# Kernel optimization log

Measured on AMD Instinct MI355X. Metric: run time of the kernel, lower is better.

The kernel has to match this reference:

```python
import math
import jax, jax.numpy as jnp
import numpy as np

H = 8
DIM = 256
HD = DIM // H
SCALE = math.sqrt(HD)
EPS = 1e-16


def _segment_softmax(scores, dst, num_nodes):
    # scores: [E, H], dst: [E] -> softmax over edges sharing the same dst
    m = jax.ops.segment_max(scores, dst, num_segments=num_nodes)  # [N, H]
    m = jnp.where(jnp.isfinite(m), m, 0.0)  # empty segments -> -inf -> 0
    e = jnp.exp(scores - m[dst])
    s = jax.ops.segment_sum(e, dst, num_segments=num_nodes)  # [N, H]
    return e / (s[dst] + EPS)


def _graph_attention(x, edges, wq, bq, wk, bk, wv, bv, wo, bo):
    # x: [N, DIM]; edges: [2, E] (src, dst). Dropout is identity (eval mode).
    N = x.shape[0]
    Q = (x @ wq + bq).reshape(N, H, HD)
    K = (x @ wk + bk).reshape(N, H, HD)
    V = (x @ wv + bv).reshape(N, H, HD)
    src, dst = edges[0], edges[1]
    scores = jnp.einsum('ehd,ehd->eh', Q[dst], K[src]) / SCALE  # [E, H]
    attn = _segment_softmax(scores, dst, N)  # [E, H]
    msgs = V[src] * attn[:, :, None]  # [E, H, HD]
    out = jax.ops.segment_sum(msgs, dst, num_segments=N).reshape(N, DIM)
    return out @ wo + bo


def _linear_params(key, fan_in, fan_out):
    k1, k2 = jax.random.split(key)
    bound = 1.0 / math.sqrt(fan_in)
    w = jax.random.uniform(k1, (fan_in, fan_out), minval=-bound, maxval=bound, dtype=jnp.float32)
    b = jax.random.uniform(k2, (fan_out,), minval=-bound, maxval=bound, dtype=jnp.float32)
    return w, b


def setup_inputs() -> dict:
    key = jax.random.key(0)
    ks = jax.random.split(key, 12)
    n_slot, n_dom = 20000, 1000
    e_slot, e_dom = 320000, 16000
    inp = {
        'slot_x': jax.random.normal(ks[0], (n_slot, DIM), dtype=jnp.float32),
        'domain_x': jax.random.normal(ks[1], (n_dom, DIM), dtype=jnp.float32),
        'slot_edges': jax.random.randint(ks[2], (2, e_slot), 0, n_slot, dtype=jnp.int32),
        'domain_edges': jax.random.randint(ks[3], (2, e_dom), 0, n_dom, dtype=jnp.int32),
    }
    names = ['wq', 'wk', 'wv', 'wo']
    for i, nm in enumerate(names):
        w, b = _linear_params(ks[4 + i], DIM, DIM)
        inp[f'slot_{nm}'] = w
        inp[f'slot_{nm}_b'] = b
    for i, nm in enumerate(names):
        w, b = _linear_params(ks[8 + i], DIM, DIM)
        inp[f'dom_{nm}'] = w
        inp[f'dom_{nm}_b'] = b
    return inp


def reference(slot_x, domain_x, slot_edges, domain_edges,
              slot_wq, slot_wq_b, slot_wk, slot_wk_b, slot_wv, slot_wv_b, slot_wo, slot_wo_b,
              dom_wq, dom_wq_b, dom_wk, dom_wk_b, dom_wv, dom_wv_b, dom_wo, dom_wo_b):
    # slot branch: self-attention on slot graph + identity residual
    slot_out = _graph_attention(slot_x, slot_edges,
                                slot_wq, slot_wq_b, slot_wk, slot_wk_b,
                                slot_wv, slot_wv_b, slot_wo, slot_wo_b) + slot_x
    # domain branch
    dom_out = _graph_attention(domain_x, domain_edges,
                               dom_wq, dom_wq_b, dom_wk, dom_wk_b,
                               dom_wv, dom_wv_b, dom_wo, dom_wo_b) + domain_x
    return slot_out, dom_out
```

## Files before the change

### kernel.cpp

```cpp
#include <hip/hip_runtime.h>
#include <hip/hip_bf16.h>

#define DIM 256
#define INV_SCALE 0.17677669529663687f
#define SM_EPS 1e-16f
#define CAP 64

typedef unsigned short ushortT;
typedef unsigned int uintT;
typedef __attribute__((ext_vector_type(8))) __bf16 bf16x8;
typedef __attribute__((ext_vector_type(4))) float f32x4;

__device__ __forceinline__ float bf2f(ushortT u) {
    return __uint_as_float(((uintT)u) << 16);
}
__device__ __forceinline__ ushortT f2bf(float f) {
    uintT u = __float_as_uint(f);
    u += 0x7FFFu + ((u >> 16) & 1u);
    return (ushortT)(u >> 16);
}

struct WPack { const void* w[8]; const void* b[8]; };

__device__ __forceinline__ bool sniff_m16(const ushortT* __restrict__ x) {
    int lane = threadIdx.x & 63;
    ushortT u = x[lane * 2];
    int e = (u >> 7) & 0xFF;
    bool sane = ((u & 0x7FFFu) == 0) || (e >= 0x66 && e <= 0x90);
    unsigned long long m = __ballot(sane);
    return __popcll(m) >= 32;
}

__global__ __launch_bounds__(256) void megaA(
        const void* __restrict__ xs, const void* __restrict__ xd,
        const ushortT* __restrict__ sniff_src,
        ushortT* __restrict__ xb_s, ushortT* __restrict__ xb_d,
        WPack pk, ushortT* __restrict__ wT, float* __restrict__ biasF,
        int* __restrict__ flagWs,
        const int* __restrict__ src_s, const int* __restrict__ dst_s,
        const int* __restrict__ src_d, const int* __restrict__ dst_d,
        int* __restrict__ cnt_s, int* __restrict__ cnt_d,
        int* __restrict__ col_s, int* __restrict__ col_d,
        int Es_, int Ed_, int nSc,
        int n4s, int n4d, int nA0, int nA1)
{
    const int bid = blockIdx.x;
    const int t = threadIdx.x;

    if (bid < nSc) {
        const int idx = bid * 256 + t;
        if (idx < Es_) {
            const int dv = dst_s[idx];
            const int pos = atomicAdd(&cnt_s[dv], 1);
            if (pos < CAP) col_s[(size_t)dv * CAP + pos] = src_s[idx];
        } else {
            const int e = idx - Es_;
            if (e < Ed_) {
                const int dv = dst_d[e];
                const int pos = atomicAdd(&cnt_d[dv], 1);
                if (pos < CAP) col_d[(size_t)dv * CAP + pos] = src_d[e];
            }
        }
        return;
    }
    const bool m16 = sniff_m16(sniff_src);
    const int li2 = bid - nSc;

    if (li2 < nA0 + nA1) {
        const bool d = li2 >= nA0;
        const int li = d ? li2 - nA0 : li2;
        const int n4 = d ? n4d : n4s;
        const int i = li * 256 + t;
        if (i >= n4) return;
        const void* x = d ? xd : xs;
        ushortT* xb = d ? xb_d : xb_s;
        if (m16) {
            ((ushort4*)xb)[i] = ((const ushort4*)x)[i];
        } else {
            float4 v = ((const float4*)x)[i];
            ushort4 o2;
            o2.x = f2bf(v.x); o2.y = f2bf(v.y); o2.z = f2bf(v.z); o2.w = f2bf(v.w);
            ((ushort4*)xb)[i] = o2;
        }
    } else if (li2 < nA0 + nA1 + 128) {
        __shared__ float sh[64][65];
        const int r0 = li2 - (nA0 + nA1);
        const int which = r0 >> 4;
        const int tile = r0 & 15;
        const int tr = tile >> 2, tc = tile & 3;
        const void* w = pk.w[which];
        const int tx = t & 63, tg = t >> 6;
        #pragma unroll
        for (int i = 0; i < 16; ++i) {
            const int r = i * 4 + tg;
            const size_t si = (size_t)(tr * 64 + r) * 256 + tc * 64 + tx;
            sh[r][tx] = m16 ? bf2f(((const ushortT*)w)[si]) : ((const float*)w)[si];
        }
        __syncthreads();
        ushortT* o = wT + (size_t)which * 65536;
        #pragma unroll
        for (int i = 0; i < 16; ++i) {
            const int r = i * 4 + tg;
            o[(size_t)(tc * 64 + r) * 256 + tr * 64 + tx] = f2bf(sh[tx][r]);
        }
    } else if (li2 < nA0 + nA1 + 136) {
        const int which = li2 - (nA0 + nA1 + 128);
        const void* b = pk.b[which];
        float v = m16 ? bf2f(((const ushortT*)b)[t]) : ((const float*)b)[t];
        biasF[which * 256 + t] = v;
    } else {
        if (t == 0) *flagWs = m16 ? 1 : 0;
    }
}

__global__ __launch_bounds__(256) void megaB(
        const ushortT* __restrict__ xb_s, const ushortT* __restrict__ xb_d,
        const ushortT* __restrict__ wT, const float* __restrict__ biasF,
        ushortT* __restrict__ qkv_s, ushortT* __restrict__ qkv_d,
        size_t zss, size_t zsd, int Ms, int Md, int nbs_, int nbq_)
{
    const int bid = blockIdx.x;
    const int by  = bid / nbq_;
    const int bx0 = bid % nbq_;
    const bool dom = bx0 >= nbs_;
    const int bx = dom ? bx0 - nbs_ : bx0;
    const ushortT* A = dom ? xb_d : xb_s;
    const int M = dom ? Md : Ms;
    const int wbase = dom ? 4 : 0;
    const size_t zstride = dom ? zsd : zss;
    ushortT* Cb = dom ? qkv_d : qkv_s;

    __shared__ ushortT As[64 * 256];

    const int tid  = threadIdx.x;
    const int wid  = tid >> 6;
    const int lane = tid & 63;
    const int m    = lane & 15;
    const int q    = lane >> 4;
    const int row0 = bx * 64;
    const int col0 = by * 64;
    const int colw = col0 + wid * 16 + m;

    {
        const int r  = tid >> 2;
        const int qt = tid & 3;
        const size_t rowAddr = (size_t)min(row0 + r, M - 1) * DIM;
        const int xr = r & 7;
        #pragma unroll
        for (int j = 0; j < 8; ++j) {
            const int chunk = qt * 8 + j;
            uint4 v = *(const uint4*)(A + rowAddr + chunk * 8);
            *(uint4*)&As[r * 256 + ((chunk ^ xr) * 8)] = v;
        }
    }

    f32x4 acc[3][4];
    #pragma unroll
    for (int z = 0; z < 3; ++z)
        #pragma unroll
        for (int i = 0; i < 4; ++i)
            acc[z][i] = (f32x4){0.f, 0.f, 0.f, 0.f};

    const ushortT* Bp = wT + (size_t)wbase * 65536 + (size_t)colw * DIM + q * 8;
    const int xm = m & 7;

    __syncthreads();

    #pragma unroll
    for (int kk = 0; kk < 8; ++kk) {
        bf16x8 bf[3];
        #pragma unroll
        for (int z = 0; z < 3; ++z)
            bf[z] = *(const bf16x8*)(Bp + (size_t)z * 65536 + kk * 32);
        bf16x8 af[4];
        #pragma unroll
        for (int i = 0; i < 4; ++i)
            af[i] = *(const bf16x8*)&As[(i * 16 + m) * 256 + (((q + 4 * kk) ^ xm) * 8)];
        #pragma unroll
        for (int z = 0; z < 3; ++z)
            #pragma unroll
            for (int i = 0; i < 4; ++i)
                acc[z][i] = __builtin_amdgcn_mfma_f32_16x16x32_bf16(bf[z], af[i], acc[z][i], 0, 0, 0);
    }

    const int colbase = col0 + wid * 16 + q * 4;
    #pragma unroll
    for (int z = 0; z < 3; ++z) {
        ushortT* C = Cb + (size_t)z * zstride;
        const float4 b4 = *(const float4*)&biasF[(wbase + z) * 256 + colbase];
        #pragma unroll
        for (int i = 0; i < 4; ++i) {
            const int row = row0 + i * 16 + m;
            if (row < M) {
                ushort4 o;
                o.x = f2bf(acc[z][i][0] + b4.x);
                o.y = f2bf(acc[z][i][1] + b4.y);
                o.z = f2bf(acc[z][i][2] + b4.z);
                o.w = f2bf(acc[z][i][3] + b4.w);
                *(ushort4*)(C + (size_t)row * DIM + colbase) = o;
            }
        }
    }
}

__global__ __launch_bounds__(256) void attn_kernel(
        const ushortT* __restrict__ Qs, const ushortT* __restrict__ Ks,
        const ushortT* __restrict__ Vs, const int* __restrict__ cnts,
        const int* __restrict__ css, ushortT* __restrict__ aggs,
        const ushortT* __restrict__ Qd_, const ushortT* __restrict__ Kd_,
        const ushortT* __restrict__ Vd_, const int* __restrict__ cntd,
        const int* __restrict__ csd, ushortT* __restrict__ aggd,
        int Ns_, int Ntot)
{
    const int g = blockIdx.x * 4 + (threadIdx.x >> 6);
    if (g >= Ntot) return;
    const bool dom = g >= Ns_;
    const int d = dom ? g - Ns_ : g;
    const int t = threadIdx.x & 63;
    const ushortT* Qb = dom ? Qd_ : Qs;
    const ushortT* Kb = dom ? Kd_ : Ks;
    const ushortT* Vb = dom ? Vd_ : Vs;
    const int* cnt = dom ? cntd : cnts;
    const int* colsrc = dom ? csd : css;
    ushortT* aggb = dom ? aggd : aggs;

    const int t4 = t * 4;
    const size_t cbase = (size_t)d * DIM + t4;
    uint2 qv = *(const uint2*)(Qb + cbase);
    const float q0 = bf2f((ushortT)(qv.x & 0xFFFF)), q1 = bf2f((ushortT)(qv.x >> 16));
    const float q2 = bf2f((ushortT)(qv.y & 0xFFFF)), q3 = bf2f((ushortT)(qv.y >> 16));

    float a0 = 0.f, a1 = 0.f, a2 = 0.f, a3 = 0.f, den = 0.f;

    auto PROC = [&](uint2 kvc, uint2 vvc) {
        float k0 = bf2f((ushortT)(kvc.x & 0xFFFF)), k1 = bf2f((ushortT)(kvc.x >> 16));
        float k2 = bf2f((ushortT)(kvc.y & 0xFFFF)), k3 = bf2f((ushortT)(kvc.y >> 16));
        float p = q0 * k0 + q1 * k1 + q2 * k2 + q3 * k3;
        p += __shfl_xor(p, 1, 8);
        p += __shfl_xor(p, 2, 8);
        p += __shfl_xor(p, 4, 8);
        const float w = __expf(fminf(p * INV_SCALE, 60.0f));
        den += w;
        a0 += w * bf2f((ushortT)(vvc.x & 0xFFFF));
        a1 += w * bf2f((ushortT)(vvc.x >> 16));
        a2 += w * bf2f((ushortT)(vvc.y & 0xFFFF));
        a3 += w * bf2f((ushortT)(vvc.y >> 16));
    };

    int deg = cnt[d];
    if (deg > CAP) deg = CAP;
    const int* cl = colsrc + (size_t)d * CAP;
    int i = 0;
    for (; i + 4 <= deg; i += 4) {
        const int s0 = cl[i], s1 = cl[i + 1];
        const int s2 = cl[i + 2], s3 = cl[i + 3];
        const size_t b0 = (size_t)s0 * DIM + t4, b1 = (size_t)s1 * DIM + t4;
        const size_t b2 = (size_t)s2 * DIM + t4, b3 = (size_t)s3 * DIM + t4;
        uint2 k0v = *(const uint2*)(Kb + b0), v0v = *(const uint2*)(Vb + b0);
        uint2 k1v = *(const uint2*)(Kb + b1), v1v = *(const uint2*)(Vb + b1);
        uint2 k2v = *(const uint2*)(Kb + b2), v2v = *(const uint2*)(Vb + b2);
        uint2 k3v = *(const uint2*)(Kb + b3), v3v = *(const uint2*)(Vb + b3);
        PROC(k0v, v0v); PROC(k1v, v1v); PROC(k2v, v2v); PROC(k3v, v3v);
    }
    for (; i < deg; ++i) {
        const size_t sb = (size_t)cl[i] * DIM + t4;
        uint2 kv = *(const uint2*)(Kb + sb);
        uint2 vv = *(const uint2*)(Vb + sb);
        PROC(kv, vv);
    }

    const float r = 1.0f / (den + SM_EPS);
    ushort4 o;
    o.x = f2bf(a0 * r); o.y = f2bf(a1 * r); o.z = f2bf(a2 * r); o.w = f2bf(a3 * r);
    *(ushort4*)(aggb + cbase) = o;
}

__global__ __launch_bounds__(256) void gemm_out(
        const ushortT* __restrict__ As_, const ushortT* __restrict__ Ad_,
        const ushortT* __restrict__ wT, const float* __restrict__ biasF,
        const void* __restrict__ xs, const void* __restrict__ xd,
        void* __restrict__ dout, int Ms, int Md, int nbs,
        const int* __restrict__ flag)
{
    const bool dom = (int)blockIdx.x >= nbs;
    const int bx = dom ? blockIdx.x - nbs : blockIdx.x;
    const ushortT* A = dom ? Ad_ : As_;
    const int M = dom ? Md : Ms;
    const int widx = 3 + (dom ? 4 : 0);
    const ushortT* BT = wT + (size_t)widx * 65536;
    const float* bias = biasF + widx * 256;
    const void* res = dom ? xd : xs;
    const size_t outOff = dom ? (size_t)Ms * DIM : 0;

    __shared__ ushortT As2[64 * 256];

    const int tid  = threadIdx.x;
    const int wid  = tid >> 6;
    const int lane = tid & 63;
    const int m    = lane & 15;
    const int q    = lane >> 4;
    const int row0 = bx * 64;
    const int col0 = blockIdx.y * 64;
    const int colw = col0 + wid * 16 + m;

    {
        const int r  = tid >> 2;
        const int qt = tid & 3;
        const size_t rowAddr = (size_t)min(row0 + r, M - 1) * DIM;
        const int xr = r & 7;
        #pragma unroll
        for (int j = 0; j < 8; ++j) {
            const int chunk = qt * 8 + j;
            uint4 v = *(const uint4*)(A + rowAddr + chunk * 8);
            *(uint4*)&As2[r * 256 + ((chunk ^ xr) * 8)] = v;
        }
    }

    f32x4 acc[4];
    #pragma unroll
    for (int i = 0; i < 4; ++i) acc[i] = (f32x4){0.f, 0.f, 0.f, 0.f};

    const ushortT* Bp = BT + (size_t)colw * DIM + q * 8;
    const int xm = m & 7;

    __syncthreads();

    #pragma unroll
    for (int kk = 0; kk < 8; ++kk) {
        bf16x8 bf = *(const bf16x8*)(Bp + kk * 32);
        bf16x8 af[4];
        #pragma unroll
        for (int i = 0; i < 4; ++i)
            af[i] = *(const bf16x8*)&As2[(i * 16 + m) * 256 + (((q + 4 * kk) ^ xm) * 8)];
        #pragma unroll
        for (int i = 0; i < 4; ++i)
            acc[i] = __builtin_amdgcn_mfma_f32_16x16x32_bf16(bf, af[i], acc[i], 0, 0, 0);
    }

    const bool m16 = (*flag != 0);
    const int colbase = col0 + wid * 16 + q * 4;
    const float4 b4 = *(const float4*)&bias[colbase];
    #pragma unroll
    for (int i = 0; i < 4; ++i) {
        const int row = row0 + i * 16 + m;
        if (row < M) {
            const size_t ridx = (size_t)row * DIM + colbase;
            float v0 = acc[i][0] + b4.x, v1 = acc[i][1] + b4.y;
            float v2 = acc[i][2] + b4.z, v3 = acc[i][3] + b4.w;
            if (m16) {
                ushort4 rv = *(const ushort4*)((const ushortT*)res + ridx);
                v0 += bf2f(rv.x); v1 += bf2f(rv.y); v2 += bf2f(rv.z); v3 += bf2f(rv.w);
                ushort4 o;
                o.x = f2bf(v0); o.y = f2bf(v1); o.z = f2bf(v2); o.w = f2bf(v3);
                *(ushort4*)((ushortT*)dout + outOff + ridx) = o;
            } else {
                float4 rv = *(const float4*)((const float*)res + ridx);
                float4 o;
                o.x = v0 + rv.x; o.y = v1 + rv.y; o.z = v2 + rv.z; o.w = v3 + rv.w;
                *(float4*)((float*)dout + outOff + ridx) = o;
            }
        }
    }
}

extern "C" void kernel_launch(void* const* d_in, const int* in_sizes, int n_in,
                              void* d_out, int out_size, void* d_ws, size_t ws_size,
                              hipStream_t stream)
{
    const void* slot_x = d_in[0];
    const void* dom_x  = d_in[1];
    const int* slot_edges = (const int*)d_in[2];
    const int* dom_edges  = (const int*)d_in[3];
    const int Ns = in_sizes[0] / DIM;
    const int Nd = in_sizes[1] / DIM;
    const int Es = in_sizes[2] / 2;
    const int Ed = in_sizes[3] / 2;

    WPack pk;
    for (int i = 0; i < 8; ++i) { pk.w[i] = d_in[4 + 2 * i]; pk.b[i] = d_in[5 + 2 * i]; }

    char* p = (char*)d_ws;
    size_t o = 0;
    auto take = [&](size_t b) { void* r = p + o; o = (o + b + 255) & ~(size_t)255; return r; };
    const size_t ndS = (size_t)Ns * DIM;
    const size_t ndD = (size_t)Nd * DIM;
    ushortT* xb_s  = (ushortT*)take(ndS * 2);
    ushortT* qkv_s = (ushortT*)take(3 * ndS * 2);
    ushortT* agg_s = (ushortT*)take(ndS * 2);
    ushortT* xb_d  = (ushortT*)take(ndD * 2);
    ushortT* qkv_d = (ushortT*)take(3 * ndD * 2);
    ushortT* agg_d = (ushortT*)take(ndD * 2);
    ushortT* wT    = (ushortT*)take(8 * 65536 * 2);
    float*   biasF = (float*)take(8 * 256 * 4);
    int* cnt_s = (int*)take((size_t)(Ns + Nd) * 4);
    int* cnt_d = cnt_s + Ns;
    int* col_s = (int*)take((size_t)Ns * CAP * 4);
    int* col_d = (int*)take((size_t)Nd * CAP * 4);
    int* flagWs = (int*)take(256);

    const int* src_s = slot_edges;
    const int* dst_s = slot_edges + Es;
    const int* src_d = dom_edges;
    const int* dst_d = dom_edges + Ed;

    const int n4s = Ns * DIM / 4, n4d = Nd * DIM / 4;
    const int nbs = (Ns + 63) / 64;
    const int nbd = (Nd + 63) / 64;
    const int nbq = nbs + nbd;

    hipMemsetAsync(cnt_s, 0, (size_t)(Ns + Nd) * 4, stream);

    const int nSc = (Es + Ed + 255) / 256;
    const int nA0 = (n4s + 255) / 256;
    const int nA1 = (n4d + 255) / 256;
    hipLaunchKernelGGL(megaA, dim3(nSc + nA0 + nA1 + 136 + 1), dim3(256), 0, stream,
                       slot_x, dom_x, (const ushortT*)slot_x, xb_s, xb_d,
                       pk, wT, biasF, flagWs,
                       src_s, dst_s, src_d, dst_d,
                       cnt_s, cnt_d, col_s, col_d,
                       Es, Ed, nSc, n4s, n4d, nA0, nA1);

    hipLaunchKernelGGL(megaB, dim3(nbq * 4), dim3(256), 0, stream,
                       xb_s, xb_d, wT, biasF, qkv_s, qkv_d, ndS, ndD,
                       Ns, Nd, nbs, nbq);

    const int Ntot = Ns + Nd;
    hipLaunchKernelGGL(attn_kernel, dim3((Ntot + 3) / 4), dim3(256), 0, stream,
                       qkv_s, qkv_s + ndS, qkv_s + 2 * ndS, cnt_s, col_s, agg_s,
                       qkv_d, qkv_d + ndD, qkv_d + 2 * ndD, cnt_d, col_d, agg_d,
                       Ns, Ntot);

    hipLaunchKernelGGL(gemm_out, dim3(nbq, DIM / 64), dim3(256), 0, stream,
                       agg_s, agg_d, wT, biasF, slot_x, dom_x, d_out,
                       Ns, Nd, nbs, flagWs);
}
```

Baseline: 232.6 us.

## Interleave K and V rows and process several edges per scatter thread

Stores K and V for each node in one contiguous 512-element row, so the attention gather reads both from adjacent memory and can share cache lines and TLB pages. The edge-bucketing part of megaA now has each thread handle four edges, which cuts the scatter block count, and uses shift-based indexing. The interleaved layout changes the GEMM epilogue write addresses, and the larger per-thread edge work may reduce atomic parallelism.

```diff
diff --git a/kernel.cpp b/kernel.cpp
--- a/kernel.cpp
+++ b/kernel.cpp
@@ -5,6 +5,7 @@
 #define INV_SCALE 0.17677669529663687f
 #define SM_EPS 1e-16f
 #define CAP 64
+#define EPT 4
 
 typedef unsigned short ushortT;
 typedef unsigned int uintT;
@@ -48,17 +49,21 @@
     const int t = threadIdx.x;
 
     if (bid < nSc) {
-        const int idx = bid * 256 + t;
-        if (idx < Es_) {
-            const int dv = dst_s[idx];
-            const int pos = atomicAdd(&cnt_s[dv], 1);
-            if (pos < CAP) col_s[(size_t)dv * CAP + pos] = src_s[idx];
-        } else {
-            const int e = idx - Es_;
-            if (e < Ed_) {
-                const int dv = dst_d[e];
-                const int pos = atomicAdd(&cnt_d[dv], 1);
-                if (pos < CAP) col_d[(size_t)dv * CAP + pos] = src_d[e];
+        const int base = bid * (256 * EPT) + t;
+        #pragma unroll
+        for (int u = 0; u < EPT; ++u) {
+            const int idx = base + u * 256;
+            if (idx < Es_) {
+                const int dv = dst_s[idx];
+                const int pos = atomicAdd(&cnt_s[dv], 1);
+                if (pos < CAP) col_s[(dv << 6) + pos] = src_s[idx];
+            } else {
+                const int e = idx - Es_;
+                if (e < Ed_) {
+                    const int dv = dst_d[e];
+                    const int pos = atomicAdd(&cnt_d[dv], 1);
+                    if (pos < CAP) col_d[(dv << 6) + pos] = src_d[e];
+                }
             }
         }
         return;
@@ -116,8 +121,9 @@
 __global__ __launch_bounds__(256) void megaB(
         const ushortT* __restrict__ xb_s, const ushortT* __restrict__ xb_d,
         const ushortT* __restrict__ wT, const float* __restrict__ biasF,
-        ushortT* __restrict__ qkv_s, ushortT* __restrict__ qkv_d,
-        size_t zss, size_t zsd, int Ms, int Md, int nbs_, int nbq_)
+        ushortT* __restrict__ q_s, ushortT* __restrict__ kv_s,
+        ushortT* __restrict__ q_d, ushortT* __restrict__ kv_d,
+        int Ms, int Md, int nbs_, int nbq_)
 {
     const int bid = blockIdx.x;
     const int by  = bid / nbq_;
@@ -127,8 +133,8 @@
     const ushortT* A = dom ? xb_d : xb_s;
     const int M = dom ? Md : Ms;
     const int wbase = dom ? 4 : 0;
-    const size_t zstride = dom ? zsd : zss;
-    ushortT* Cb = dom ? qkv_d : qkv_s;
+    ushortT* Q = dom ? q_d : q_s;
+    ushortT* KV = dom ? kv_d : kv_s;
 
     __shared__ ushortT As[64 * 256];
 
@@ -186,7 +192,6 @@
     const int colbase = col0 + wid * 16 + q * 4;
     #pragma unroll
     for (int z = 0; z < 3; ++z) {
-        ushortT* C = Cb + (size_t)z * zstride;
         const float4 b4 = *(const float4*)&biasF[(wbase + z) * 256 + colbase];
         #pragma unroll
         for (int i = 0; i < 4; ++i) {
@@ -197,19 +202,22 @@
                 o.y = f2bf(acc[z][i][1] + b4.y);
                 o.z = f2bf(acc[z][i][2] + b4.z);
                 o.w = f2bf(acc[z][i][3] + b4.w);
-                *(ushort4*)(C + (size_t)row * DIM + colbase) = o;
+                ushortT* C = (z == 0)
+                    ? (Q + (size_t)row * DIM + colbase)
+                    : (KV + (size_t)row * 512 + (z - 1) * 256 + colbase);
+                *(ushort4*)C = o;
             }
         }
     }
 }
 
 __global__ __launch_bounds__(256) void attn_kernel(
-        const ushortT* __restrict__ Qs, const ushortT* __restrict__ Ks,
-        const ushortT* __restrict__ Vs, const int* __restrict__ cnts,
-        const int* __restrict__ css, ushortT* __restrict__ aggs,
-        const ushortT* __restrict__ Qd_, const ushortT* __restrict__ Kd_,
-        const ushortT* __restrict__ Vd_, const int* __restrict__ cntd,
-        const int* __restrict__ csd, ushortT* __restrict__ aggd,
+        const ushortT* __restrict__ Qs, const ushortT* __restrict__ KVs,
+        const int* __restrict__ cnts, const int* __restrict__ css,
+        ushortT* __restrict__ aggs,
+        const ushortT* __restrict__ Qd_, const ushortT* __restrict__ KVd_,
+        const int* __restrict__ cntd, const int* __restrict__ csd,
+        ushortT* __restrict__ aggd,
         int Ns_, int Ntot)
 {
     const int g = blockIdx.x * 4 + (threadIdx.x >> 6);
@@ -218,8 +226,7 @@
     const int d = dom ? g - Ns_ : g;
     const int t = threadIdx.x & 63;
     const ushortT* Qb = dom ? Qd_ : Qs;
-    const ushortT* Kb = dom ? Kd_ : Ks;
-    const ushortT* Vb = dom ? Vd_ : Vs;
+    const ushortT* KVb = dom ? KVd_ : KVs;
     const int* cnt = dom ? cntd : cnts;
     const int* colsrc = dom ? csd : css;
     ushortT* aggb = dom ? aggd : aggs;
@@ -249,23 +256,23 @@
 
     int deg = cnt[d];
     if (deg > CAP) deg = CAP;
-    const int* cl = colsrc + (size_t)d * CAP;
+    const int* cl = colsrc + ((size_t)d << 6);
     int i = 0;
     for (; i + 4 <= deg; i += 4) {
         const int s0 = cl[i], s1 = cl[i + 1];
         const int s2 = cl[i + 2], s3 = cl[i + 3];
-        const size_t b0 = (size_t)s0 * DIM + t4, b1 = (size_t)s1 * DIM + t4;
-        const size_t b2 = (size_t)s2 * DIM + t4, b3 = (size_t)s3 * DIM + t4;
-        uint2 k0v = *(const uint2*)(Kb + b0), v0v = *(const uint2*)(Vb + b0);
-        uint2 k1v = *(const uint2*)(Kb + b1), v1v = *(const uint2*)(Vb + b1);
-        uint2 k2v = *(const uint2*)(Kb + b2), v2v = *(const uint2*)(Vb + b2);
-        uint2 k3v = *(const uint2*)(Kb + b3), v3v = *(const uint2*)(Vb + b3);
+        const size_t b0 = ((size_t)s0 << 9) + t4, b1 = ((size_t)s1 << 9) + t4;
+        const size_t b2 = ((size_t)s2 << 9) + t4, b3 = ((size_t)s3 << 9) + t4;
+        uint2 k0v = *(const uint2*)(KVb + b0), v0v = *(const uint2*)(KVb + b0 + 256);
+        uint2 k1v = *(const uint2*)(KVb + b1), v1v = *(const uint2*)(KVb + b1 + 256);
+        uint2 k2v = *(const uint2*)(KVb + b2), v2v = *(const uint2*)(KVb + b2 + 256);
+        uint2 k3v = *(const uint2*)(KVb + b3), v3v = *(const uint2*)(KVb + b3 + 256);
         PROC(k0v, v0v); PROC(k1v, v1v); PROC(k2v, v2v); PROC(k3v, v3v);
     }
     for (; i < deg; ++i) {
-        const size_t sb = (size_t)cl[i] * DIM + t4;
-        uint2 kv = *(const uint2*)(Kb + sb);
-        uint2 vv = *(const uint2*)(Vb + sb);
+        const size_t sb = ((size_t)cl[i] << 9) + t4;
+        uint2 kv = *(const uint2*)(KVb + sb);
+        uint2 vv = *(const uint2*)(KVb + sb + 256);
         PROC(kv, vv);
     }
 
@@ -385,10 +392,12 @@
     const size_t ndS = (size_t)Ns * DIM;
     const size_t ndD = (size_t)Nd * DIM;
     ushortT* xb_s  = (ushortT*)take(ndS * 2);
-    ushortT* qkv_s = (ushortT*)take(3 * ndS * 2);
+    ushortT* q_s   = (ushortT*)take(ndS * 2);
+    ushortT* kv_s  = (ushortT*)take(2 * ndS * 2);
     ushortT* agg_s = (ushortT*)take(ndS * 2);
     ushortT* xb_d  = (ushortT*)take(ndD * 2);
-    ushortT* qkv_d = (ushortT*)take(3 * ndD * 2);
+    ushortT* q_d   = (ushortT*)take(ndD * 2);
+    ushortT* kv_d  = (ushortT*)take(2 * ndD * 2);
     ushortT* agg_d = (ushortT*)take(ndD * 2);
     ushortT* wT    = (ushortT*)take(8 * 65536 * 2);
     float*   biasF = (float*)take(8 * 256 * 4);
@@ -410,7 +419,8 @@
 
     hipMemsetAsync(cnt_s, 0, (size_t)(Ns + Nd) * 4, stream);
 
-    const int nSc = (Es + Ed + 255) / 256;
+    const int Etot = Es + Ed;
+    const int nSc = (Etot + 256 * EPT - 1) / (256 * EPT);
     const int nA0 = (n4s + 255) / 256;
     const int nA1 = (n4d + 255) / 256;
     hipLaunchKernelGGL(megaA, dim3(nSc + nA0 + nA1 + 136 + 1), dim3(256), 0, stream,
@@ -421,13 +431,13 @@
                        Es, Ed, nSc, n4s, n4d, nA0, nA1);
 
     hipLaunchKernelGGL(megaB, dim3(nbq * 4), dim3(256), 0, stream,
-                       xb_s, xb_d, wT, biasF, qkv_s, qkv_d, ndS, ndD,
+                       xb_s, xb_d, wT, biasF, q_s, kv_s, q_d, kv_d,
                        Ns, Nd, nbs, nbq);
 
     const int Ntot = Ns + Nd;
     hipLaunchKernelGGL(attn_kernel, dim3((Ntot + 3) / 4), dim3(256), 0, stream,
-                       qkv_s, qkv_s + ndS, qkv_s + 2 * ndS, cnt_s, col_s, agg_s,
-                       qkv_d, qkv_d + ndD, qkv_d + 2 * ndD, cnt_d, col_d, agg_d,
+                       q_s, kv_s, cnt_s, col_s, agg_s,
+                       q_d, kv_d, cnt_d, col_d, agg_d,
                        Ns, Ntot);
 
     hipLaunchKernelGGL(gemm_out, dim3(nbq, DIM / 64), dim3(256), 0, stream,
```

Result: no change. 231.6 us (-0.4%).
